# Kernel tuning notes

Measured on AMD Instinct MI355X. Metric: run time of the kernel, lower is better.

## Reference

```python
import jax, jax.numpy as jnp
import numpy as np

B, N, S, K, D = 8, 16384, 1024, 32, 64
MLP = [64, 64, 128]
C_IN = 3 + D  # grouped_xyz_norm (3) concat grouped point features (D)
EPS = 1e-5


def setup_inputs() -> dict:
    key = jax.random.key(0)
    ks = jax.random.split(key, 16)
    inp = {
        "xyz": jax.random.normal(ks[0], (B, 3, N), dtype=jnp.float32),
        "points": jax.random.normal(ks[1], (B, D, N), dtype=jnp.float32),
        "sample_idx": jax.random.randint(ks[2], (B, S), 0, N, dtype=jnp.int32),
    }
    last = C_IN
    for i, oc in enumerate(MLP):
        scale = 1.0 / np.sqrt(last)
        inp[f"w{i}"] = jax.random.uniform(ks[3 + 4 * i], (oc, last), jnp.float32, -scale, scale)
        inp[f"b{i}"] = jax.random.uniform(ks[4 + 4 * i], (oc,), jnp.float32, -scale, scale)
        inp[f"g{i}"] = jnp.ones((oc,), jnp.float32)   # BN gamma
        inp[f"be{i}"] = jnp.zeros((oc,), jnp.float32)  # BN beta
        last = oc
    return inp


def _gather(pts, idx):
    # pts: [B,N,C], idx: [B,...] -> [B,...,C]
    return jax.vmap(lambda p, i: p[i])(pts, idx)


def _mlp_layer(x, w, b, g, be):
    # x: [B,C,K,S]; 1x1 Conv2d + BatchNorm2d (training-mode batch stats) + ReLU
    y = jnp.einsum("bcks,oc->boks", x, w) + b[None, :, None, None]
    mu = jnp.mean(y, axis=(0, 2, 3), keepdims=True)
    var = jnp.var(y, axis=(0, 2, 3), keepdims=True)
    y = (y - mu) * jax.lax.rsqrt(var + EPS)
    y = y * g[None, :, None, None] + be[None, :, None, None]
    return jax.nn.relu(y)


def reference(xyz, points, sample_idx, w0, b0, g0, be0, w1, b1, g1, be1, w2, b2, g2, be2):
    xyz_t = jnp.transpose(xyz, (0, 2, 1))      # [B,N,3]
    pts_t = jnp.transpose(points, (0, 2, 1))   # [B,N,D]
    idx_s = sample_idx.astype(jnp.int32)

    new_xyz = _gather(xyz_t, idx_s)            # [B,S,3]

    # square_distance(new_xyz, xyz): [B,S,N]
    d = (jnp.sum(new_xyz ** 2, -1)[:, :, None]
         + jnp.sum(xyz_t ** 2, -1)[:, None, :]
         - 2.0 * jnp.einsum("bsc,bnc->bsn", new_xyz, xyz_t))
    _, idx = jax.lax.top_k(-d, K)              # kNN indices [B,S,K]

    grouped_xyz = _gather(xyz_t, idx)          # [B,S,K,3]
    grouped_norm = grouped_xyz - new_xyz[:, :, None, :]
    grouped_pts = _gather(pts_t, idx)          # [B,S,K,D]
    feat = jnp.concatenate([grouped_norm, grouped_pts], axis=-1)  # [B,S,K,3+D]

    x = jnp.transpose(feat, (0, 3, 2, 1))      # [B,C,K,S]
    x = _mlp_layer(x, w0, b0, g0, be0)
    x = _mlp_layer(x, w1, b1, g1, be1)
    x = _mlp_layer(x, w2, b2, g2, be2)
    new_points = jnp.max(x, axis=2)            # [B,128,S]

    return (jnp.transpose(new_xyz, (0, 2, 1)), new_points, grouped_xyz, idx_s)
```

## Files before the change

### kernel.cpp

```cpp
#include <hip/hip_runtime.h>

constexpr int cB = 8, cN = 16384, cS = 1024, cK = 32, cD = 64;
constexpr int cO2 = 128;
constexpr int PTOT = cB * cS * cK;
constexpr int NBLK2 = PTOT / 128;

constexpr int OUT1_OFF = cB * 3 * cS;
constexpr int OUT2_OFF = OUT1_OFF + cB * cO2 * cS;
constexpr int OUT3_OFF = OUT2_OFF + cB * cS * cK * 3;

constexpr size_t WS_PTS  = 0;
constexpr size_t WS_XYZP = WS_PTS  + (size_t)cB * cN * cD * 4;
constexpr size_t WS_IDX  = WS_XYZP + (size_t)cB * cN * 16;
constexpr size_t WS_NORM = WS_IDX  + (size_t)PTOT * 4;
constexpr size_t WS_Y0   = WS_NORM + (size_t)PTOT * 3 * 4;
constexpr size_t WS_Y1   = WS_Y0   + (size_t)PTOT * 64 * 4;
constexpr size_t WS_MX   = WS_Y1   + (size_t)PTOT * 64 * 4;
constexpr size_t WS_MN   = WS_MX   + (size_t)cB * cS * cO2 * 4;
constexpr size_t WS_P0   = WS_MN   + (size_t)cB * cS * cO2 * 4;
constexpr size_t WS_P1   = WS_P0   + (size_t)NBLK2 * 64 * 8;
constexpr size_t WS_P2   = WS_P1   + (size_t)NBLK2 * 64 * 8;
constexpr size_t WS_BN   = WS_P2   + (size_t)NBLK2 * 128 * 8;
constexpr size_t WS_END  = WS_BN   + 3 * 128 * 2 * 4;

__device__ __forceinline__ unsigned keyOf(float d) {
    unsigned u = __float_as_uint(d);
    return u ^ ((unsigned)((int)u >> 31) | 0x80000000u);
}
__device__ __forceinline__ float distNp(float qx, float qy, float qz, float sq, float4 p) {
    float m0 = __fmul_rn(qx, p.x);
    float m1 = __fmul_rn(qy, p.y);
    float m2 = __fmul_rn(qz, p.z);
    float dt = __fadd_rn(__fadd_rn(m0, m1), m2);
    return __fsub_rn(__fadd_rn(sq, p.w), __fmul_rn(2.0f, dt));
}

__global__ __launch_bounds__(256) void k_prep(const float* __restrict__ pts,
                                              const float* __restrict__ xyz,
                                              float* __restrict__ ptsT,
                                              float4* __restrict__ xyzp) {
    __shared__ float tile[64][65];
    int blk = blockIdx.x;
    int tid = threadIdx.x;
    if (blk < 2048) {
        int b = blk >> 8;
        int n0 = (blk & 255) * 64;
        for (int it = 0; it < 16; ++it) {
            int l = it * 256 + tid;
            int c = l >> 6, nn = l & 63;
            tile[nn][c] = pts[((size_t)b * 64 + c) * cN + n0 + nn];
        }
        __syncthreads();
        for (int it = 0; it < 16; ++it) {
            int l = it * 256 + tid;
            int nn = l >> 6, c = l & 63;
            ptsT[((size_t)(b * cN + n0 + nn)) * 64 + c] = tile[nn][c];
        }
    } else {
        int i = (blk - 2048) * 256 + tid;
        int b = i >> 14, n = i & (cN - 1);
        float x = xyz[(b * 3 + 0) * cN + n];
        float y = xyz[(b * 3 + 1) * cN + n];
        float z = xyz[(b * 3 + 2) * cN + n];
        float sq = __fadd_rn(__fadd_rn(__fmul_rn(x, x), __fmul_rn(y, y)), __fmul_rn(z, z));
        xyzp[i] = make_float4(x, y, z, sq);
    }
}

#define QB 8
#define CAP 256

__device__ __forceinline__ void selectBin2(const unsigned* __restrict__ h, int lane,
                                           int target, int* Tout, int* cbOut) {
    int base = lane * 8;
    unsigned hh[8];
    unsigned c8 = 0;
#pragma unroll
    for (int i = 0; i < 8; i++) { hh[i] = h[base + i]; c8 += hh[i]; }
    unsigned incl = c8;
#pragma unroll
    for (int off = 1; off < 32; off <<= 1) {
        unsigned t = __shfl_up(incl, (unsigned)off, 32);
        if (lane >= off) incl += t;
    }
    int excl = (int)(incl - c8);
    if (excl < target && target <= (int)incl) {
        int c = excl;
#pragma unroll
        for (int i = 0; i < 8; i++) {
            int nc = c + (int)hh[i];
            if (c < target && target <= nc) { *Tout = base + i; *cbOut = c; }
            c = nc;
        }
    }
}

__global__ __launch_bounds__(256, 4) void k_knn(const float* __restrict__ xyz,
                                                const int* __restrict__ sidx_g,
                                                const float4* __restrict__ xyzp,
                                                int* __restrict__ idxw,
                                                float* __restrict__ normw,
                                                float* __restrict__ outbuf) {
    __shared__ unsigned hist[QB][258];
    __shared__ unsigned long long cand[QB][CAP];
    __shared__ unsigned cnt[QB];
    __shared__ float qxs[QB], qys[QB], qzs[QB], sqs[QB];
    __shared__ int sIdx[QB];
    __shared__ float s1s[QB], tAs[QB], tBs[QB];
    __shared__ int T1s[QB], cb1s[QB], T2s[QB], cb2s[QB];
    __shared__ float tAcc[QB];
    __shared__ int refq[QB];
    __shared__ int anyRef;
    __shared__ unsigned order[QB][cK];

    int tid = threadIdx.x;
    int qi = tid >> 5, lane = tid & 31;
    int qbase = blockIdx.x * QB;
    int b = qbase / cS;
    int s0 = qbase % cS;
    const float4* pb = xyzp + (size_t)b * cN;

    if (tid < QB) {
        int si = sidx_g[b * cS + s0 + tid];
        sIdx[tid] = si;
        float x = xyz[(b * 3 + 0) * cN + si];
        float y = xyz[(b * 3 + 1) * cN + si];
        float z = xyz[(b * 3 + 2) * cN + si];
        qxs[tid] = x; qys[tid] = y; qzs[tid] = z;
        sqs[tid] = __fadd_rn(__fadd_rn(__fmul_rn(x, x), __fmul_rn(y, y)), __fmul_rn(z, z));
        cnt[tid] = 0u;
    }
    if (tid == 0) anyRef = 0;
    for (int i = tid; i < QB * 258; i += 256) ((unsigned*)hist)[i] = 0u;
    __syncthreads();

    {
        float qx = qxs[qi], qy = qys[qi], qz = qzs[qi], qsq = sqs[qi];
        float dmin = 3.4e38f;
        for (int t = 0; t < 64; ++t) {
            float4 p = pb[lane + 32 * t];
            float dot = fmaf(qx, p.x, fmaf(qy, p.y, qz * p.z));
            float d = fmaf(-2.0f, dot, qsq + p.w);
            dmin = fminf(dmin, d);
        }
        float rmax = dmin;
#pragma unroll
        for (int off = 16; off; off >>= 1)
            rmax = fmaxf(rmax, __shfl_xor(rmax, off, 32));
        if (lane == 0) {
            float R = fmaxf(rmax, 1e-12f);
            float s1 = 254.0f / R;
            s1s[qi] = s1;
            tAs[qi] = qsq * s1;
            tBs[qi] = -2.0f * s1;
        }
    }
    __syncthreads();

    float lqx[QB], lqy[QB], lqz[QB], lS[QB], lA[QB], lB[QB];
#pragma unroll
    for (int q = 0; q < QB; q++) {
        lqx[q] = qxs[q]; lqy[q] = qys[q]; lqz[q] = qzs[q];
        lS[q] = s1s[q]; lA[q] = tAs[q]; lB[q] = tBs[q];
    }

    for (int j = 0; j < cN / 256; ++j) {
        float4 p = pb[j * 256 + tid];
#pragma unroll
        for (int q = 0; q < QB; ++q) {
            float dot = fmaf(lqx[q], p.x, fmaf(lqy[q], p.y, lqz[q] * p.z));
            float t = fmaf(dot, lB[q], fmaf(p.w, lS[q], lA[q]));
            if (t < 258.0f) {
                int bin = __float2int_rz(fmaxf(t, 0.0f));
                atomicAdd(&hist[q][bin], 1u);
            }
        }
    }
    __syncthreads();

    selectBin2(hist[qi], lane, cK, &T1s[qi], &cb1s[qi]);
    __syncthreads();
    if (tid < QB) {
        int T1 = T1s[tid];
        int acc = cb1s[tid] + (int)hist[tid][T1] + (int)hist[tid][T1 + 1];
        int nr = (acc > CAP) ? 1 : 0;
        refq[tid] = nr;
        tAcc[tid] = (float)(T1 + 2);
        if (nr) atomicOr(&anyRef, 1);
    }
    __syncthreads();

    if (anyRef) {
        for (int i = tid; i < QB * 258; i += 256) ((unsigned*)hist)[i] = 0u;
        __syncthreads();
        int lT1[QB], lrf[QB];
#pragma unroll
        for (int q = 0; q < QB; q++) { lT1[q] = T1s[q]; lrf[q] = refq[q]; }
        for (int j = 0; j < cN / 256; ++j) {
            float4 p = pb[j * 256 + tid];
#pragma unroll
            for (int q = 0; q < QB; ++q) {
                if (lrf[q]) {
                    float dot = fmaf(lqx[q], p.x, fmaf(lqy[q], p.y, lqz[q] * p.z));
                    float t = fmaf(dot, lB[q], fmaf(p.w, lS[q], lA[q]));
                    float um = fmaxf(t, 0.0f) - (float)lT1[q];
                    if (um >= 0.0f && um < 2.0f) {
                        int sub = min(255, __float2int_rz(um * 128.0f));
                        atomicAdd(&hist[q][sub], 1u);
                    }
                }
            }
        }
        __syncthreads();
        if (refq[qi]) selectBin2(hist[qi], lane, cK - cb1s[qi], &T2s[qi], &cb2s[qi]);
        __syncthreads();
        if (tid < QB && refq[tid])
            tAcc[tid] = (float)T1s[tid] + (float)(T2s[tid] + 2) * 0.0078125f;
        __syncthreads();
    }

    float lsq[QB], lt[QB];
#pragma unroll
    for (int q = 0; q < QB; q++) { lsq[q] = sqs[q]; lt[q] = tAcc[q]; }

    for (int j = 0; j < cN / 256; ++j) {
        int n = j * 256 + tid;
        float4 p = pb[n];
#pragma unroll
        for (int q = 0; q < QB; ++q) {
            float dot = fmaf(lqx[q], p.x, fmaf(lqy[q], p.y, lqz[q] * p.z));
            float t = fmaf(dot, lB[q], fmaf(p.w, lS[q], lA[q]));
            if (t < lt[q]) {
                float de = distNp(lqx[q], lqy[q], lqz[q], lsq[q], p);
                unsigned pos = atomicAdd(&cnt[q], 1u);
                if (pos < CAP)
                    cand[q][pos] = ((unsigned long long)keyOf(de) << 32) | (unsigned)n;
            }
        }
    }
    __syncthreads();

    int m = (int)min(cnt[qi], (unsigned)CAP);
    for (int r = 0; r < cK; ++r) {
        unsigned long long best = ~0ull;
        int bslot = -1;
        for (int i = lane; i < m; i += 32) {
            unsigned long long v = cand[qi][i];
            if (v < best) { best = v; bslot = i; }
        }
#pragma unroll
        for (int off = 16; off; off >>= 1) {
            unsigned long long ov = __shfl_xor(best, off, 32);
            int os = __shfl_xor(bslot, off, 32);
            if (ov < best) { best = ov; bslot = os; }
        }
        if (lane == 0) {
            order[qi][r] = (best != ~0ull) ? (unsigned)(best & 0xFFFFFFFFull) : 0u;
            if (bslot >= 0) cand[qi][bslot] = ~0ull;
        }
    }

    {
        int r = lane;
        int s = s0 + qi;
        int n = (int)order[qi][r];
        size_t pos = (size_t)(b * cS + s) * cK + r;
        idxw[pos] = n;
        float px = xyz[(b * 3 + 0) * cN + n];
        float py = xyz[(b * 3 + 1) * cN + n];
        float pz = xyz[(b * 3 + 2) * cN + n];
        outbuf[OUT2_OFF + pos * 3 + 0] = px;
        outbuf[OUT2_OFF + pos * 3 + 1] = py;
        outbuf[OUT2_OFF + pos * 3 + 2] = pz;
        normw[pos * 3 + 0] = __fsub_rn(px, qxs[qi]);
        normw[pos * 3 + 1] = __fsub_rn(py, qys[qi]);
        normw[pos * 3 + 2] = __fsub_rn(pz, qzs[qi]);
        if (r == 0) {
            outbuf[OUT3_OFF + b * cS + s] = (float)sIdx[qi];
            outbuf[(b * 3 + 0) * cS + s] = qxs[qi];
            outbuf[(b * 3 + 1) * cS + s] = qys[qi];
            outbuf[(b * 3 + 2) * cS + s] = qzs[qi];
        }
    }
}

__global__ __launch_bounds__(256) void k_conv0(const int* __restrict__ idxw,
                                               const float* __restrict__ normw,
                                               const float* __restrict__ ptsT,
                                               const float* __restrict__ w0,
                                               const float* __restrict__ b0,
                                               float* __restrict__ y0,
                                               float2* __restrict__ part0) {
    __shared__ __align__(16) float fAT[67 * 132];
    __shared__ __align__(16) float wT[67 * 68];
    __shared__ float bl[64];
    int tid = threadIdx.x;
    int blk = blockIdx.x;
    int b = blk >> 8;
    int s0 = (blk & 255) << 2;
    size_t posbase = ((size_t)b * cS + s0) * cK;

    for (int l = tid; l < 64 * 67; l += 256) {
        int o = l / 67, c = l - o * 67;
        wT[c * 68 + o] = w0[l];
    }
    if (tid < 64) bl[tid] = b0[tid];
    {
        int r = tid >> 1, half = tid & 1;
        size_t pos = posbase + r;
        int n = idxw[pos];
        const float* pr = ptsT + ((size_t)b * cN + n) * 64 + half * 32;
#pragma unroll
        for (int q = 0; q < 8; q++) {
            float4 v = *(const float4*)(pr + q * 4);
            int c = 3 + half * 32 + q * 4;
            fAT[(c + 0) * 132 + r] = v.x;
            fAT[(c + 1) * 132 + r] = v.y;
            fAT[(c + 2) * 132 + r] = v.z;
            fAT[(c + 3) * 132 + r] = v.w;
        }
        if (half == 0) {
            fAT[0 * 132 + r] = normw[pos * 3 + 0];
            fAT[1 * 132 + r] = normw[pos * 3 + 1];
            fAT[2 * 132 + r] = normw[pos * 3 + 2];
        }
    }
    __syncthreads();

    int ry = tid >> 4, tx = tid & 15;
    float acc[8][4];
#pragma unroll
    for (int i = 0; i < 8; i++)
#pragma unroll
        for (int j = 0; j < 4; j++) acc[i][j] = bl[tx * 4 + j];

    for (int c = 0; c < 67; ++c) {
        const float* fb = fAT + c * 132;
        float4 a0 = *(const float4*)(fb + ry * 8);
        float4 a1 = *(const float4*)(fb + ry * 8 + 4);
        float4 wv = *(const float4*)&wT[c * 68 + tx * 4];
        float av[8] = {a0.x, a0.y, a0.z, a0.w, a1.x, a1.y, a1.z, a1.w};
#pragma unroll
        for (int i = 0; i < 8; i++) {
            acc[i][0] = fmaf(av[i], wv.x, acc[i][0]);
            acc[i][1] = fmaf(av[i], wv.y, acc[i][1]);
            acc[i][2] = fmaf(av[i], wv.z, acc[i][2]);
            acc[i][3] = fmaf(av[i], wv.w, acc[i][3]);
        }
    }
#pragma unroll
    for (int i = 0; i < 8; i++) {
        float4 o4 = make_float4(acc[i][0], acc[i][1], acc[i][2], acc[i][3]);
        *(float4*)(y0 + (posbase + ry * 8 + i) * 64 + tx * 4) = o4;
    }
    __syncthreads();

    float* ps = wT;
    float* pq = wT + 16 * 64;
#pragma unroll
    for (int j = 0; j < 4; j++) {
        float s = 0.f, q = 0.f;
#pragma unroll
        for (int i = 0; i < 8; i++) { float v = acc[i][j]; s += v; q += v * v; }
        ps[ry * 64 + tx * 4 + j] = s;
        pq[ry * 64 + tx * 4 + j] = q;
    }
    __syncthreads();
    if (tid < 64) {
        float s = 0.f, q = 0.f;
        for (int t = 0; t < 16; t++) { s += ps[t * 64 + tid]; q += pq[t * 64 + tid]; }
        part0[(size_t)blk * 64 + tid] = make_float2(s, q);
    }
}

__global__ __launch_bounds__(256) void k_conv1(const float* __restrict__ yin,
                                               const float2* __restrict__ bnin,
                                               const float* __restrict__ w,
                                               const float* __restrict__ bb,
                                               float* __restrict__ yout,
                                               float2* __restrict__ part) {
    __shared__ __align__(16) float fAT[64 * 132];
    __shared__ __align__(16) float wT[64 * 68];
    __shared__ float bl[64], al[64], sl[64];
    int tid = threadIdx.x;
    int blk = blockIdx.x;
    int b = blk >> 8;
    int s0 = (blk & 255) << 2;
    size_t posbase = ((size_t)b * cS + s0) * cK;

    if (tid < 64) {
        bl[tid] = bb[tid];
        float2 t = bnin[tid];
        al[tid] = t.x; sl[tid] = t.y;
    }
    __syncthreads();
    for (int l = tid; l < 64 * 64; l += 256) {
        int o = l >> 6, c = l & 63;
        wT[c * 68 + o] = w[l];
    }
    {
        int r = tid >> 1, half = tid & 1;
        const float* yr = yin + (posbase + r) * 64 + half * 32;
#pragma unroll
        for (int q = 0; q < 8; q++) {
            float4 v = *(const float4*)(yr + q * 4);
            int c = half * 32 + q * 4;
            v.x = fmaxf(fmaf(v.x, al[c + 0], sl[c + 0]), 0.0f);
            v.y = fmaxf(fmaf(v.y, al[c + 1], sl[c + 1]), 0.0f);
            v.z = fmaxf(fmaf(v.z, al[c + 2], sl[c + 2]), 0.0f);
            v.w = fmaxf(fmaf(v.w, al[c + 3], sl[c + 3]), 0.0f);
            fAT[(c + 0) * 132 + r] = v.x;
            fAT[(c + 1) * 132 + r] = v.y;
            fAT[(c + 2) * 132 + r] = v.z;
            fAT[(c + 3) * 132 + r] = v.w;
        }
    }
    __syncthreads();

    int ry = tid >> 4, tx = tid & 15;
    float acc[8][4];
#pragma unroll
    for (int i = 0; i < 8; i++)
#pragma unroll
        for (int j = 0; j < 4; j++) acc[i][j] = bl[tx * 4 + j];

    for (int c = 0; c < 64; ++c) {
        const float* fb = fAT + c * 132;
        float4 a0 = *(const float4*)(fb + ry * 8);
        float4 a1 = *(const float4*)(fb + ry * 8 + 4);
        float4 wv = *(const float4*)&wT[c * 68 + tx * 4];
        float av[8] = {a0.x, a0.y, a0.z, a0.w, a1.x, a1.y, a1.z, a1.w};
#pragma unroll
        for (int i = 0; i < 8; i++) {
            acc[i][0] = fmaf(av[i], wv.x, acc[i][0]);
            acc[i][1] = fmaf(av[i], wv.y, acc[i][1]);
            acc[i][2] = fmaf(av[i], wv.z, acc[i][2]);
            acc[i][3] = fmaf(av[i], wv.w, acc[i][3]);
        }
    }
#pragma unroll
    for (int i = 0; i < 8; i++) {
        float4 o4 = make_float4(acc[i][0], acc[i][1], acc[i][2], acc[i][3]);
        *(float4*)(yout + (posbase + ry * 8 + i) * 64 + tx * 4) = o4;
    }
    __syncthreads();

    float* ps = wT;
    float* pq = wT + 16 * 64;
#pragma unroll
    for (int j = 0; j < 4; j++) {
        float s = 0.f, q = 0.f;
#pragma unroll
        for (int i = 0; i < 8; i++) { float v = acc[i][j]; s += v; q += v * v; }
        ps[ry * 64 + tx * 4 + j] = s;
        pq[ry * 64 + tx * 4 + j] = q;
    }
    __syncthreads();
    if (tid < 64) {
        float s = 0.f, q = 0.f;
        for (int t = 0; t < 16; t++) { s += ps[t * 64 + tid]; q += pq[t * 64 + tid]; }
        part[(size_t)blk * 64 + tid] = make_float2(s, q);
    }
}

__global__ __launch_bounds__(256) void k_conv2(const float* __restrict__ y1,
                                               const float2* __restrict__ bn1,
                                               const float* __restrict__ w2,
                                               const float* __restrict__ b2,
                                               float* __restrict__ mx,
                                               float* __restrict__ mn,
                                               float2* __restrict__ part2) {
    __shared__ __align__(16) float fAT[64 * 132];
    __shared__ __align__(16) float wT[64 * 132];
    __shared__ float al[64], sl[64], bl[128];
    int tid = threadIdx.x;
    int blk = blockIdx.x;
    int b = blk >> 8;
    int s0 = (blk & 255) << 2;
    size_t posbase = ((size_t)b * cS + s0) * cK;

    if (tid < 64) { float2 t = bn1[tid]; al[tid] = t.x; sl[tid] = t.y; }
    if (tid < 128) bl[tid] = b2[tid];
    __syncthreads();

    {
        int r = tid >> 1, half = tid & 1;
        const float* yr = y1 + (posbase + r) * 64 + half * 32;
#pragma unroll
        for (int q = 0; q < 8; q++) {
            float4 v = *(const float4*)(yr + q * 4);
            int c = half * 32 + q * 4;
            v.x = fmaxf(fmaf(v.x, al[c + 0], sl[c + 0]), 0.0f);
            v.y = fmaxf(fmaf(v.y, al[c + 1], sl[c + 1]), 0.0f);
            v.z = fmaxf(fmaf(v.z, al[c + 2], sl[c + 2]), 0.0f);
            v.w = fmaxf(fmaf(v.w, al[c + 3], sl[c + 3]), 0.0f);
            fAT[(c + 0) * 132 + r] = v.x;
            fAT[(c + 1) * 132 + r] = v.y;
            fAT[(c + 2) * 132 + r] = v.z;
            fAT[(c + 3) * 132 + r] = v.w;
        }
    }
    for (int l = tid; l < 128 * 64; l += 256) {
        int o = l >> 6, c = l & 63;
        wT[c * 132 + o] = w2[l];
    }
    __syncthreads();

    int ry = tid >> 4, tx = tid & 15;
    float acc[8][8];
#pragma unroll
    for (int i = 0; i < 8; i++) {
#pragma unroll
        for (int j = 0; j < 4; j++) acc[i][j] = bl[tx * 4 + j];
#pragma unroll
        for (int j = 4; j < 8; j++) acc[i][j] = bl[64 + tx * 4 + (j - 4)];
    }

    for (int c = 0; c < 64; ++c) {
        const float* fb = fAT + c * 132;
        const float* wb = wT + c * 132;
        float4 a0 = *(const float4*)(fb + ry * 8);
        float4 a1 = *(const float4*)(fb + ry * 8 + 4);
        float4 w0v = *(const float4*)(wb + tx * 4);
        float4 w1v = *(const float4*)(wb + 64 + tx * 4);
        float av[8] = {a0.x, a0.y, a0.z, a0.w, a1.x, a1.y, a1.z, a1.w};
        float wv[8] = {w0v.x, w0v.y, w0v.z, w0v.w, w1v.x, w1v.y, w1v.z, w1v.w};
#pragma unroll
        for (int i = 0; i < 8; i++)
#pragma unroll
            for (int j = 0; j < 8; j++)
                acc[i][j] = fmaf(av[i], wv[j], acc[i][j]);
    }
    __syncthreads();

    float* ps  = wT;
    float* pq  = wT + 16 * 128;
    float* pmx = wT + 32 * 128;
    float* pmn = wT + 48 * 128;
#pragma unroll
    for (int j = 0; j < 8; j++) {
        int o = (j < 4) ? (tx * 4 + j) : (64 + tx * 4 + (j - 4));
        float s = 0.f, q = 0.f;
        float mv = -3.402823466e+38f, nv = 3.402823466e+38f;
#pragma unroll
        for (int i = 0; i < 8; i++) {
            float v = acc[i][j];
            s += v; q += v * v;
            mv = fmaxf(mv, v); nv = fminf(nv, v);
        }
        ps[ry * 128 + o] = s;
        pq[ry * 128 + o] = q;
        pmx[ry * 128 + o] = mv;
        pmn[ry * 128 + o] = nv;
    }
    __syncthreads();
    if (tid < 128) {
        float s = 0.f, q = 0.f;
        for (int t = 0; t < 16; t++) { s += ps[t * 128 + tid]; q += pq[t * 128 + tid]; }
        part2[(size_t)blk * 128 + tid] = make_float2(s, q);
    }
    for (int e = tid; e < 512; e += 256) {
        int sg = e >> 7, o = e & 127;
        float mv = -3.402823466e+38f, nv = 3.402823466e+38f;
        for (int t = sg * 4; t < sg * 4 + 4; ++t) {
            mv = fmaxf(mv, pmx[t * 128 + o]);
            nv = fminf(nv, pmn[t * 128 + o]);
        }
        int s = s0 + sg;
        mx[((size_t)b * cS + s) * 128 + o] = mv;
        mn[((size_t)b * cS + s) * 128 + o] = nv;
    }
}

__global__ __launch_bounds__(256) void k_fin(const float2* __restrict__ part, int nblk,
                                             int oc,
                                             const float* __restrict__ g,
                                             const float* __restrict__ be,
                                             float2* __restrict__ bnout) {
    __shared__ double rs[256], rq[256];
    int o = blockIdx.x;
    int tid = threadIdx.x;
    double s = 0.0, q = 0.0;
    for (int i = tid; i < nblk; i += 256) {
        float2 p = part[(size_t)i * oc + o];
        s += (double)p.x;
        q += (double)p.y;
    }
    rs[tid] = s; rq[tid] = q;
    __syncthreads();
    for (int off = 128; off; off >>= 1) {
        if (tid < off) { rs[tid] += rs[tid + off]; rq[tid] += rq[tid + off]; }
        __syncthreads();
    }
    if (tid == 0) {
        double cntv = (double)PTOT;
        double mu = rs[0] / cntv;
        double var = rq[0] / cntv - mu * mu;
        if (var < 0.0) var = 0.0;
        float a = (float)((double)g[o] / sqrt(var + 1e-5));
        float sh = (float)((double)be[o] - mu * (double)a);
        bnout[o] = make_float2(a, sh);
    }
}

__global__ __launch_bounds__(256) void k_final(const float* __restrict__ mx,
                                               const float* __restrict__ mn,
                                               const float2* __restrict__ bn2,
                                               float* __restrict__ out1) {
    int i = blockIdx.x * 256 + threadIdx.x;
    int b = i >> 17;
    int r = i & ((1 << 17) - 1);
    int o = r >> 10;
    int s = r & 1023;
    float2 t = bn2[o];
    size_t idx = ((size_t)b * cS + s) * 128 + o;
    float M = (t.x >= 0.0f) ? mx[idx] : mn[idx];
    out1[i] = fmaxf(t.x * M + t.y, 0.0f);
}

extern "C" void kernel_launch(void* const* d_in, const int* in_sizes, int n_in,
                              void* d_out, int out_size, void* d_ws, size_t ws_size,
                              hipStream_t stream) {
    (void)in_sizes; (void)n_in; (void)out_size;
    const float* xyz = (const float*)d_in[0];
    const float* pts = (const float*)d_in[1];
    const int* sidx  = (const int*)d_in[2];
    const float* w0  = (const float*)d_in[3];
    const float* b0  = (const float*)d_in[4];
    const float* g0  = (const float*)d_in[5];
    const float* be0 = (const float*)d_in[6];
    const float* w1  = (const float*)d_in[7];
    const float* b1  = (const float*)d_in[8];
    const float* g1  = (const float*)d_in[9];
    const float* be1 = (const float*)d_in[10];
    const float* w2  = (const float*)d_in[11];
    const float* b2  = (const float*)d_in[12];
    const float* g2  = (const float*)d_in[13];
    const float* be2 = (const float*)d_in[14];
    float* out = (float*)d_out;
    char* ws = (char*)d_ws;
    if (ws_size < WS_END) return;

    float* ptsT  = (float*)(ws + WS_PTS);
    float4* xyzp = (float4*)(ws + WS_XYZP);
    int* idxw    = (int*)(ws + WS_IDX);
    float* normw = (float*)(ws + WS_NORM);
    float* y0    = (float*)(ws + WS_Y0);
    float* y1    = (float*)(ws + WS_Y1);
    float* mx    = (float*)(ws + WS_MX);
    float* mn    = (float*)(ws + WS_MN);
    float2* p0   = (float2*)(ws + WS_P0);
    float2* p1   = (float2*)(ws + WS_P1);
    float2* p2   = (float2*)(ws + WS_P2);
    float2* bnb  = (float2*)(ws + WS_BN);

    hipLaunchKernelGGL(k_prep, dim3(2048 + cB * cN / 256), dim3(256), 0, stream,
                       pts, xyz, ptsT, xyzp);
    hipLaunchKernelGGL(k_knn, dim3(cB * cS / QB), dim3(256), 0, stream,
                       xyz, sidx, xyzp, idxw, normw, out);
    hipLaunchKernelGGL(k_conv0, dim3(NBLK2), dim3(256), 0, stream,
                       idxw, normw, ptsT, w0, b0, y0, p0);
    hipLaunchKernelGGL(k_fin, dim3(64), dim3(256), 0, stream, p0, NBLK2, 64, g0, be0, bnb);
    hipLaunchKernelGGL(k_conv1, dim3(NBLK2), dim3(256), 0, stream, y0, bnb, w1, b1, y1, p1);
    hipLaunchKernelGGL(k_fin, dim3(64), dim3(256), 0, stream, p1, NBLK2, 64, g1, be1, bnb + 128);
    hipLaunchKernelGGL(k_conv2, dim3(NBLK2), dim3(256), 0, stream,
                       y1, bnb + 128, w2, b2, mx, mn, p2);
    hipLaunchKernelGGL(k_fin, dim3(128), dim3(256), 0, stream, p2, NBLK2, 128, g2, be2, bnb + 256);
    hipLaunchKernelGGL(k_final, dim3(cB * cO2 * cS / 256), dim3(256), 0, stream,
                       mx, mn, bnb + 256, out + OUT1_OFF);
}
```

Measured before the change: 380.4 us.

## Recompute conv0 inside conv1 instead of storing y0 to global memory

Layer-0 conv becomes a stats-only pass that no longer writes y0. A new fused kernel regathers the input features, recomputes conv0, applies BN0 and ReLU in registers, stages the result in shared memory and runs conv1 directly. This removes the write and read of the 64-channel y0 tensor (PTOT*64 floats each way). The cost is a second gather of the point features and a second conv0 GEMM, plus larger shared-memory use in the fused kernel.

```diff
diff --git a/kernel.cpp b/kernel.cpp
--- a/kernel.cpp
+++ b/kernel.cpp
@@ -13,8 +13,7 @@
 constexpr size_t WS_XYZP = WS_PTS  + (size_t)cB * cN * cD * 4;
 constexpr size_t WS_IDX  = WS_XYZP + (size_t)cB * cN * 16;
 constexpr size_t WS_NORM = WS_IDX  + (size_t)PTOT * 4;
-constexpr size_t WS_Y0   = WS_NORM + (size_t)PTOT * 3 * 4;
-constexpr size_t WS_Y1   = WS_Y0   + (size_t)PTOT * 64 * 4;
+constexpr size_t WS_Y1   = WS_NORM + (size_t)PTOT * 3 * 4;
 constexpr size_t WS_MX   = WS_Y1   + (size_t)PTOT * 64 * 4;
 constexpr size_t WS_MN   = WS_MX   + (size_t)cB * cS * cO2 * 4;
 constexpr size_t WS_P0   = WS_MN   + (size_t)cB * cS * cO2 * 4;
@@ -284,13 +283,12 @@
     }
 }
 
-__global__ __launch_bounds__(256) void k_conv0(const int* __restrict__ idxw,
-                                               const float* __restrict__ normw,
-                                               const float* __restrict__ ptsT,
-                                               const float* __restrict__ w0,
-                                               const float* __restrict__ b0,
-                                               float* __restrict__ y0,
-                                               float2* __restrict__ part0) {
+__global__ __launch_bounds__(256) void k_conv0s(const int* __restrict__ idxw,
+                                                const float* __restrict__ normw,
+                                                const float* __restrict__ ptsT,
+                                                const float* __restrict__ w0,
+                                                const float* __restrict__ b0,
+                                                float2* __restrict__ part0) {
     __shared__ __align__(16) float fAT[67 * 132];
     __shared__ __align__(16) float wT[67 * 68];
     __shared__ float bl[64];
@@ -348,11 +346,6 @@
             acc[i][3] = fmaf(av[i], wv.w, acc[i][3]);
         }
     }
-#pragma unroll
-    for (int i = 0; i < 8; i++) {
-        float4 o4 = make_float4(acc[i][0], acc[i][1], acc[i][2], acc[i][3]);
-        *(float4*)(y0 + (posbase + ry * 8 + i) * 64 + tx * 4) = o4;
-    }
     __syncthreads();
 
     float* ps = wT;
@@ -373,46 +366,53 @@
     }
 }
 
-__global__ __launch_bounds__(256) void k_conv1(const float* __restrict__ yin,
-                                               const float2* __restrict__ bnin,
-                                               const float* __restrict__ w,
-                                               const float* __restrict__ bb,
-                                               float* __restrict__ yout,
-                                               float2* __restrict__ part) {
-    __shared__ __align__(16) float fAT[64 * 132];
-    __shared__ __align__(16) float wT[64 * 68];
-    __shared__ float bl[64], al[64], sl[64];
+__global__ __launch_bounds__(256) void k_conv01(const int* __restrict__ idxw,
+                                                const float* __restrict__ normw,
+                                                const float* __restrict__ ptsT,
+                                                const float* __restrict__ w0,
+                                                const float* __restrict__ b0,
+                                                const float2* __restrict__ bn0,
+                                                const float* __restrict__ w1,
+                                                const float* __restrict__ b1,
+                                                float* __restrict__ y1,
+                                                float2* __restrict__ part1) {
+    __shared__ __align__(16) float fU[8704];
+    __shared__ __align__(16) float wbuf[67 * 68];
+    __shared__ float bl0[64], al[64], sl[64], bl1[64];
     int tid = threadIdx.x;
     int blk = blockIdx.x;
     int b = blk >> 8;
     int s0 = (blk & 255) << 2;
     size_t posbase = ((size_t)b * cS + s0) * cK;
 
+    for (int l = tid; l < 64 * 67; l += 256) {
+        int o = l / 67, c = l - o * 67;
+        wbuf[c * 68 + o] = w0[l];
+    }
     if (tid < 64) {
-        bl[tid] = bb[tid];
-        float2 t = bnin[tid];
+        bl0[tid] = b0[tid];
+        float2 t = bn0[tid];
         al[tid] = t.x; sl[tid] = t.y;
-    }
-    __syncthreads();
-    for (int l = tid; l < 64 * 64; l += 256) {
-        int o = l >> 6, c = l & 63;
-        wT[c * 68 + o] = w[l];
+        bl1[tid] = b1[tid];
     }
     {
         int r = tid >> 1, half = tid & 1;
-        const float* yr = yin + (posbase + r) * 64 + half * 32;
+        size_t pos = posbase + r;
+        int n = idxw[pos];
+        const float* pr = ptsT + ((size_t)b * cN + n) * 64 + half * 32;
 #pragma unroll
         for (int q = 0; q < 8; q++) {
-            float4 v = *(const float4*)(yr + q * 4);
-            int c = half * 32 + q * 4;
-            v.x = fmaxf(fmaf(v.x, al[c + 0], sl[c + 0]), 0.0f);
-            v.y = fmaxf(fmaf(v.y, al[c + 1], sl[c + 1]), 0.0f);
-            v.z = fmaxf(fmaf(v.z, al[c + 2], sl[c + 2]), 0.0f);
-            v.w = fmaxf(fmaf(v.w, al[c + 3], sl[c + 3]), 0.0f);
-            fAT[(c + 0) * 132 + r] = v.x;
-            fAT[(c + 1) * 132 + r] = v.y;
-            fAT[(c + 2) * 132 + r] = v.z;
-            fAT[(c + 3) * 132 + r] = v.w;
+            float4 v = *(const float4*)(pr + q * 4);
+            int c = 3 + half * 32 + q * 4;
+            fU[(c + 0) * 128 + r] = v.x;
+            fU[(c + 1) * 128 + r] = v.y;
+            fU[(c + 2) * 128 + r] = v.z;
+            fU[(c + 3) * 128 + r] = v.w;
+        }
+        if (half == 0) {
+            fU[0 * 128 + r] = normw[pos * 3 + 0];
+            fU[1 * 128 + r] = normw[pos * 3 + 1];
+            fU[2 * 128 + r] = normw[pos * 3 + 2];
         }
     }
     __syncthreads();
@@ -422,13 +422,13 @@
 #pragma unroll
     for (int i = 0; i < 8; i++)
 #pragma unroll
-        for (int j = 0; j < 4; j++) acc[i][j] = bl[tx * 4 + j];
-
-    for (int c = 0; c < 64; ++c) {
-        const float* fb = fAT + c * 132;
+        for (int j = 0; j < 4; j++) acc[i][j] = bl0[tx * 4 + j];
+
+    for (int c = 0; c < 67; ++c) {
+        const float* fb = fU + c * 128;
         float4 a0 = *(const float4*)(fb + ry * 8);
         float4 a1 = *(const float4*)(fb + ry * 8 + 4);
-        float4 wv = *(const float4*)&wT[c * 68 + tx * 4];
+        float4 wv = *(const float4*)&wbuf[c * 68 + tx * 4];
         float av[8] = {a0.x, a0.y, a0.z, a0.w, a1.x, a1.y, a1.z, a1.w};
 #pragma unroll
         for (int i = 0; i < 8; i++) {
@@ -438,20 +438,70 @@
             acc[i][3] = fmaf(av[i], wv.w, acc[i][3]);
         }
     }
+    __syncthreads();
+
+    for (int l = tid; l < 64 * 64; l += 256) {
+        int o = l >> 6, c = l & 63;
+        wbuf[c * 68 + o] = w1[l];
+    }
 #pragma unroll
     for (int i = 0; i < 8; i++) {
-        float4 o4 = make_float4(acc[i][0], acc[i][1], acc[i][2], acc[i][3]);
-        *(float4*)(yout + (posbase + ry * 8 + i) * 64 + tx * 4) = o4;
-    }
-    __syncthreads();
-
-    float* ps = wT;
-    float* pq = wT + 16 * 64;
+        int row = ry * 8 + i;
+        float4 v;
+        v.x = fmaxf(fmaf(acc[i][0], al[tx * 4 + 0], sl[tx * 4 + 0]), 0.0f);
+        v.y = fmaxf(fmaf(acc[i][1], al[tx * 4 + 1], sl[tx * 4 + 1]), 0.0f);
+        v.z = fmaxf(fmaf(acc[i][2], al[tx * 4 + 2], sl[tx * 4 + 2]), 0.0f);
+        v.w = fmaxf(fmaf(acc[i][3], al[tx * 4 + 3], sl[tx * 4 + 3]), 0.0f);
+        *(float4*)&fU[row * 68 + tx * 4] = v;
+    }
+    __syncthreads();
+
+    float acc1[8][4];
+#pragma unroll
+    for (int i = 0; i < 8; i++)
+#pragma unroll
+        for (int j = 0; j < 4; j++) acc1[i][j] = bl1[tx * 4 + j];
+
+    for (int c4 = 0; c4 < 16; ++c4) {
+        float4 wv[4];
+#pragma unroll
+        for (int cc = 0; cc < 4; cc++)
+            wv[cc] = *(const float4*)&wbuf[(c4 * 4 + cc) * 68 + tx * 4];
+#pragma unroll
+        for (int i = 0; i < 8; i++) {
+            float4 a = *(const float4*)&fU[(ry * 8 + i) * 68 + c4 * 4];
+            acc1[i][0] = fmaf(a.x, wv[0].x, acc1[i][0]);
+            acc1[i][1] = fmaf(a.x, wv[0].y, acc1[i][1]);
+            acc1[i][2] = fmaf(a.x, wv[0].z, acc1[i][2]);
+            acc1[i][3] = fmaf(a.x, wv[0].w, acc1[i][3]);
+            acc1[i][0] = fmaf(a.y, wv[1].x, acc1[i][0]);
+            acc1[i][1] = fmaf(a.y, wv[1].y, acc1[i][1]);
+            acc1[i][2] = fmaf(a.y, wv[1].z, acc1[i][2]);
+            acc1[i][3] = fmaf(a.y, wv[1].w, acc1[i][3]);
+            acc1[i][0] = fmaf(a.z, wv[2].x, acc1[i][0]);
+            acc1[i][1] = fmaf(a.z, wv[2].y, acc1[i][1]);
+            acc1[i][2] = fmaf(a.z, wv[2].z, acc1[i][2]);
+            acc1[i][3] = fmaf(a.z, wv[2].w, acc1[i][3]);
+            acc1[i][0] = fmaf(a.w, wv[3].x, acc1[i][0]);
+            acc1[i][1] = fmaf(a.w, wv[3].y, acc1[i][1]);
+            acc1[i][2] = fmaf(a.w, wv[3].z, acc1[i][2]);
+            acc1[i][3] = fmaf(a.w, wv[3].w, acc1[i][3]);
+        }
+    }
+#pragma unroll
+    for (int i = 0; i < 8; i++) {
+        float4 o4 = make_float4(acc1[i][0], acc1[i][1], acc1[i][2], acc1[i][3]);
+        *(float4*)(y1 + (posbase + ry * 8 + i) * 64 + tx * 4) = o4;
+    }
+    __syncthreads();
+
+    float* ps = wbuf;
+    float* pq = wbuf + 16 * 64;
 #pragma unroll
     for (int j = 0; j < 4; j++) {
         float s = 0.f, q = 0.f;
 #pragma unroll
-        for (int i = 0; i < 8; i++) { float v = acc[i][j]; s += v; q += v * v; }
+        for (int i = 0; i < 8; i++) { float v = acc1[i][j]; s += v; q += v * v; }
         ps[ry * 64 + tx * 4 + j] = s;
         pq[ry * 64 + tx * 4 + j] = q;
     }
@@ -459,7 +509,7 @@
     if (tid < 64) {
         float s = 0.f, q = 0.f;
         for (int t = 0; t < 16; t++) { s += ps[t * 64 + tid]; q += pq[t * 64 + tid]; }
-        part[(size_t)blk * 64 + tid] = make_float2(s, q);
+        part1[(size_t)blk * 64 + tid] = make_float2(s, q);
     }
 }
 
@@ -645,7 +695,6 @@
     float4* xyzp = (float4*)(ws + WS_XYZP);
     int* idxw    = (int*)(ws + WS_IDX);
     float* normw = (float*)(ws + WS_NORM);
-    float* y0    = (float*)(ws + WS_Y0);
     float* y1    = (float*)(ws + WS_Y1);
     float* mx    = (float*)(ws + WS_MX);
     float* mn    = (float*)(ws + WS_MN);
@@ -658,10 +707,11 @@
                        pts, xyz, ptsT, xyzp);
     hipLaunchKernelGGL(k_knn, dim3(cB * cS / QB), dim3(256), 0, stream,
                        xyz, sidx, xyzp, idxw, normw, out);
-    hipLaunchKernelGGL(k_conv0, dim3(NBLK2), dim3(256), 0, stream,
-                       idxw, normw, ptsT, w0, b0, y0, p0);
+    hipLaunchKernelGGL(k_conv0s, dim3(NBLK2), dim3(256), 0, stream,
+                       idxw, normw, ptsT, w0, b0, p0);
     hipLaunchKernelGGL(k_fin, dim3(64), dim3(256), 0, stream, p0, NBLK2, 64, g0, be0, bnb);
-    hipLaunchKernelGGL(k_conv1, dim3(NBLK2), dim3(256), 0, stream, y0, bnb, w1, b1, y1, p1);
+    hipLaunchKernelGGL(k_conv01, dim3(NBLK2), dim3(256), 0, stream,
+                       idxw, normw, ptsT, w0, b0, bnb, w1, b1, y1, p1);
     hipLaunchKernelGGL(k_fin, dim3(64), dim3(256), 0, stream, p1, NBLK2, 64, g1, be1, bnb + 128);
     hipLaunchKernelGGL(k_conv2, dim3(NBLK2), dim3(256), 0, stream,
                        y1, bnb + 128, w2, b2, mx, mn, p2);
```

Measured after the change: 407.5 us. +7.1%, slower.
